# Kernel tuning notes

Measured on AMD Instinct MI355X. Metric: run time of the kernel, lower is better.

Reference implementation:

```python
import jax, jax.numpy as jnp
import numpy as np

NUM_HEADS = 8


def setup_inputs() -> dict:
    key = jax.random.key(0)
    ks = jax.random.split(key, 9)
    B, S, E = 16, 2048, 768
    s = 0.02
    return {
        "features": jax.random.normal(ks[0], (B, S, E), jnp.float32),
        "in_proj_w": jax.random.normal(ks[1], (3 * E, E), jnp.float32) * s,
        "in_proj_b": jnp.zeros((3 * E,), jnp.float32),
        "out_proj_w": jax.random.normal(ks[2], (E, E), jnp.float32) * s,
        "out_proj_b": jnp.zeros((E,), jnp.float32),
        "w1": jax.random.normal(ks[3], (384, E), jnp.float32) * s,
        "b1": jnp.zeros((384,), jnp.float32),
        "w2": jax.random.normal(ks[4], (1, 384), jnp.float32) * s,
        "b2": jnp.zeros((1,), jnp.float32),
    }


def reference(features, in_proj_w, in_proj_b, out_proj_w, out_proj_b, w1, b1, w2, b2):
    # torch nn.MultiheadAttention default batch_first=False: dim 0 is the
    # attended sequence axis (length B here), dim 1 is the MHA batch (S).
    B, S, E = features.shape
    H = NUM_HEADS
    Dh = E // H
    qkv = features @ in_proj_w.T + in_proj_b          # (B, S, 3E)
    q, k, v = jnp.split(qkv, 3, axis=-1)
    q = q.reshape(B, S, H, Dh)
    k = k.reshape(B, S, H, Dh)
    v = v.reshape(B, S, H, Dh)
    scale = 1.0 / jnp.sqrt(jnp.asarray(Dh, features.dtype))
    # attention over axis-0 positions (l, m in 0..B-1), per (s, h)
    scores = jnp.einsum('lshd,mshd->shlm', q * scale, k)
    attn = jax.nn.softmax(scores, axis=-1)
    ctx = jnp.einsum('shlm,mshd->lshd', attn, v).reshape(B, S, E)
    attn_out = ctx @ out_proj_w.T + out_proj_b        # (B, S, E)
    # batched 2-layer MLP (replaces the Python per-row loop)
    h = jax.nn.relu(attn_out @ w1.T + b1)             # (B, S, 384)
    prob = h @ w2.T + b2                              # (B, S, 1)
    contacts = jnp.broadcast_to(prob, (B, S, S))      # contacts[:, i, :] = prob[:, i]
    return contacts
```

## Files before the change

kernel.cpp:

```cpp
#include <hip/hip_runtime.h>

typedef unsigned short u16;
typedef __attribute__((ext_vector_type(8))) __bf16 bf16x8;
typedef __attribute__((ext_vector_type(4))) float floatx4;

#define B_DIM  16
#define S_DIM  2048
#define E_DIM  768
#define HEADS  8
#define DHEAD  96
#define MROWS  32768
#define QKV_LD 2304
#define NT     12

#define GLDS(gp, lp) __builtin_amdgcn_global_load_lds( \
    (const __attribute__((address_space(1))) void*)(gp), \
    (__attribute__((address_space(3))) void*)(lp), 16, 0, 0)

__device__ __forceinline__ u16 f2b(float f) {
    unsigned u = __float_as_uint(f);
    u += 0x7fffu + ((u >> 16) & 1u);
    return (u16)(u >> 16);
}
__device__ __forceinline__ float blo(unsigned u) { return __uint_as_float(u << 16); }

__device__ __forceinline__ bf16x8 ldsw(const u16* half_base, int rowh, int cb) {
    return *(const bf16x8*)((const char*)half_base + rowh * 128 + (cb ^ ((rowh & 7) << 4)));
}

#define PB0 24576
#define PB1 26304
#define PB2 26592
#define PB3 27168
#define PB4 27552
__global__ __launch_bounds__(256) void prep(const float* __restrict__ features,
                                            const float* __restrict__ in_proj_w,
                                            const float* __restrict__ w1,
                                            const float* __restrict__ out_proj_w,
                                            const float* __restrict__ bo,
                                            const float* __restrict__ b1,
                                            u16* __restrict__ fbf, u16* __restrict__ wib,
                                            u16* __restrict__ w1b, u16* __restrict__ WoT,
                                            float* __restrict__ cbuf) {
    __shared__ float tsh[32][33];
    const int b = blockIdx.x, tid = threadIdx.x;
    if (b < PB2) {
        const float* src; u16* dst; long i;
        if (b < PB0)      { src = features;  dst = fbf; i = (long)b * 256 + tid; }
        else if (b < PB1) { src = in_proj_w; dst = wib; i = (long)(b - PB0) * 256 + tid; }
        else              { src = w1;        dst = w1b; i = (long)(b - PB1) * 256 + tid; }
        float4 f = ((const float4*)src)[i];
        ushort4 r;
        r.x = f2b(f.x); r.y = f2b(f.y); r.z = f2b(f.z); r.w = f2b(f.w);
        ((ushort4*)dst)[i] = r;
    } else if (b < PB3) {
        const int t = b - PB2;
        const int bxT = t % 24, byT = t / 24;
        const int tx = tid & 31, ty = tid >> 5;
        int x = bxT * 32 + tx;
        int y = byT * 32 + ty;
#pragma unroll
        for (int j = 0; j < 4; j++) tsh[ty + j * 8][tx] = out_proj_w[(long)(y + j * 8) * 768 + x];
        __syncthreads();
        x = byT * 32 + tx;
        y = bxT * 32 + ty;
#pragma unroll
        for (int j = 0; j < 4; j++) WoT[(long)(y + j * 8) * 768 + x] = f2b(tsh[tx][ty + j * 8]);
    } else {
        const int n = b - PB3;
        const float* row = w1 + (long)n * 768;
        float s = row[tid] * bo[tid] + row[tid + 256] * bo[tid + 256] + row[tid + 512] * bo[tid + 512];
#pragma unroll
        for (int off = 32; off > 0; off >>= 1) s += __shfl_xor(s, off);
        if ((tid & 63) == 0) tsh[0][tid >> 6] = s;
        __syncthreads();
        if (tid == 0) cbuf[n] = tsh[0][0] + tsh[0][1] + tsh[0][2] + tsh[0][3] + b1[n];
    }
}

__global__ __launch_bounds__(512, 2) void qkv256(const u16* __restrict__ A,
                                                 const u16* __restrict__ W,
                                                 const float* __restrict__ bias,
                                                 u16* __restrict__ Cout,
                                                 const u16* __restrict__ gA,
                                                 const u16* __restrict__ gW,
                                                 u16* __restrict__ gC) {
    __shared__ __align__(16) u16 lds[2 * 32768];
    const int tid = threadIdx.x;
    const int bx  = blockIdx.x;
    int bm, bn, ldc, Mvalid; const u16 *Aa, *Ww; const float* bs; u16* Co; bool perm;
    if (bx < 6) {
        bn = bx % 3; bm = bx / 3;
        Aa = gA; Ww = gW; bs = nullptr; Co = gC; ldc = 768; perm = false; Mvalid = 384;
    } else {
        const int xcd = bx & 7;
        const int q   = (bx >> 3) - ((bx & 7) < 6 ? 1 : 0);
        bn = q % 9;
        bm = (q / 9) * 8 + xcd;
        Aa = A; Ww = W; bs = bias; Co = Cout; ldc = QKV_LD; perm = true; Mvalid = 1 << 30;
    }
    const int r0 = tid >> 3,        r1 = (tid + 512) >> 3;
    const int q0 = (tid & 7) ^ (r0 & 7), q1 = ((tid + 512) & 7) ^ (r1 & 7);
    const u16* pA0 = Aa + (long)(bm * 256 + r0) * 768 + q0 * 8;
    const u16* pA1 = Aa + (long)(bm * 256 + r1) * 768 + q1 * 8;
    const u16* pB0 = Ww + (long)(bn * 256 + r0) * 768 + q0 * 8;
    const u16* pB1 = Ww + (long)(bn * 256 + r1) * 768 + q1 * 8;
    u16* dA0 = lds + tid * 8;
    u16* dA1 = lds + 4096 + tid * 8;
    u16* dB0 = lds + 16384 + tid * 8;
    u16* dB1 = lds + 16384 + 4096 + tid * 8;

#define IS_A(h, p, t) do { \
    GLDS(pA0 + (h) * 98304 + (t) * 64, dA0 + (p) * 32768 + (h) * 8192); \
    GLDS(pA1 + (h) * 98304 + (t) * 64, dA1 + (p) * 32768 + (h) * 8192); } while (0)
#define IS_B(h, p, t) do { \
    GLDS(pB0 + (h) * 98304 + (t) * 64, dB0 + (p) * 32768 + (h) * 8192); \
    GLDS(pB1 + (h) * 98304 + (t) * 64, dB1 + (p) * 32768 + (h) * 8192); } while (0)
#define MFMA_PRE() do { \
    __builtin_amdgcn_s_barrier(); \
    asm volatile("s_waitcnt lgkmcnt(0)" ::: "memory"); \
    __builtin_amdgcn_sched_barrier(0); \
    __builtin_amdgcn_s_setprio(1); } while (0)
#define MFMA_POST() do { \
    __builtin_amdgcn_s_setprio(0); \
    __builtin_amdgcn_s_barrier(); } while (0)

    const int lane = tid & 63, wid = tid >> 6;
    const int wr = wid >> 2, wc = wid & 3;
    const int fr = lane & 15, fg = lane >> 4;
    const int fq2 = fg * 16;
    const int wb  = (wc & 1) * 64;
    const u16* bufA_base = lds + wr * 8192;
    const u16* bufB_base = lds + 16384 + (wc >> 1) * 8192;

    IS_A(0, 0, 0); IS_A(1, 0, 0); IS_B(0, 0, 0); IS_B(1, 0, 0);
    IS_A(0, 1, 1); IS_A(1, 1, 1);
    asm volatile("s_waitcnt vmcnt(4)" ::: "memory");
    __builtin_amdgcn_s_barrier();

    floatx4 acc[8][4] = {};
#pragma unroll 2
    for (int t = 0; t < NT; ++t) {
        const int p = t & 1, pn = p ^ 1;
        const u16* bA = bufA_base + p * 32768;
        const u16* bB = bufB_base + p * 32768;
        bf16x8 aF[4], bF[4];
#pragma unroll
        for (int i = 0; i < 4; ++i) aF[i] = ldsw(bA, i * 16 + fr, fq2);
#pragma unroll
        for (int j = 0; j < 4; ++j) bF[j] = ldsw(bB, wb + j * 16 + fr, fq2);
        if (t + 1 < NT) IS_B(0, pn, t + 1);
        MFMA_PRE();
#pragma unroll
        for (int i = 0; i < 4; ++i)
#pragma unroll
            for (int j = 0; j < 4; ++j)
                acc[i][j] = __builtin_amdgcn_mfma_f32_16x16x32_bf16(aF[i], bF[j], acc[i][j], 0, 0, 0);
        MFMA_POST();
#pragma unroll
        for (int i = 0; i < 4; ++i) aF[i] = ldsw(bA, (i + 4) * 16 + fr, fq2);
        if (t + 1 < NT) IS_B(1, pn, t + 1);
        MFMA_PRE();
#pragma unroll
        for (int i = 0; i < 4; ++i)
#pragma unroll
            for (int j = 0; j < 4; ++j)
                acc[i + 4][j] = __builtin_amdgcn_mfma_f32_16x16x32_bf16(aF[i], bF[j], acc[i + 4][j], 0, 0, 0);
        MFMA_POST();
#pragma unroll
        for (int i = 0; i < 4; ++i) aF[i] = ldsw(bA, i * 16 + fr, 64 + fq2);
#pragma unroll
        for (int j = 0; j < 4; ++j) bF[j] = ldsw(bB, wb + j * 16 + fr, 64 + fq2);
        MFMA_PRE();
#pragma unroll
        for (int i = 0; i < 4; ++i)
#pragma unroll
            for (int j = 0; j < 4; ++j)
                acc[i][j] = __builtin_amdgcn_mfma_f32_16x16x32_bf16(aF[i], bF[j], acc[i][j], 0, 0, 0);
        MFMA_POST();
#pragma unroll
        for (int i = 0; i < 4; ++i) aF[i] = ldsw(bA, (i + 4) * 16 + fr, 64 + fq2);
        MFMA_PRE();
#pragma unroll
        for (int i = 0; i < 4; ++i)
#pragma unroll
            for (int j = 0; j < 4; ++j)
                acc[i + 4][j] = __builtin_amdgcn_mfma_f32_16x16x32_bf16(aF[i], bF[j], acc[i + 4][j], 0, 0, 0);
        MFMA_POST();
        if (t + 2 < NT) {
            IS_A(0, p, t + 2); IS_A(1, p, t + 2);
            asm volatile("s_waitcnt vmcnt(4)" ::: "memory");
            __builtin_amdgcn_s_barrier();
        } else if (t + 1 < NT) {
            asm volatile("s_waitcnt vmcnt(0)" ::: "memory");
            __builtin_amdgcn_s_barrier();
        }
    }

    const int rq = fg * 4;
    float bvj[4];
#pragma unroll
    for (int j = 0; j < 4; ++j) bvj[j] = bs ? bs[bn * 256 + wc * 64 + j * 16 + fr] : 0.f;
    u16* strip = lds + wid * 2304;
    const int sr = lane >> 3, sc = lane & 7;
#pragma unroll
    for (int pass = 0; pass < 4; ++pass) {
#pragma unroll
        for (int ii = 0; ii < 2; ++ii) {
            const int i = pass * 2 + ii;
#pragma unroll
            for (int j = 0; j < 4; ++j)
#pragma unroll
                for (int r = 0; r < 4; ++r)
                    strip[(ii * 16 + rq + r) * 72 + j * 16 + fr] = f2b(acc[i][j][r] + bvj[j]);
        }
#pragma unroll
        for (int it = 0; it < 4; ++it) {
            const int lr = it * 8 + sr;
            uint4 v = *(const uint4*)(strip + lr * 72 + sc * 8);
            const int rl = bm * 256 + wr * 128 + pass * 32 + lr;
            if (rl < Mvalid) {
                const long grow = perm ? (long)(((rl & 2047) << 4) | (rl >> 11)) : (long)rl;
                *(uint4*)(Co + grow * ldc + bn * 256 + wc * 64 + sc * 8) = v;
            }
        }
    }
#undef IS_A
#undef IS_B
#undef MFMA_PRE
#undef MFMA_POST
}

__global__ __launch_bounds__(256) void attn_kernel(u16* __restrict__ qkv) {
    __shared__ __align__(16) u16 sQKV[3 * 16 * 384];
    __shared__ __align__(16) u16 sP[4][2][16][16];
    const int tid = threadIdx.x;
    const int bx  = blockIdx.x;
    const int xcd   = bx & 7;
    const int hh    = (bx >> 3) & 1;
    const int inner = bx >> 4;
    const int s = (xcd << 8) | inner;
    const u16* base = qkv + (long)s * 16 * QKV_LD + hh * 384;

#pragma unroll
    for (int it = 0; it < 9; it++) {
        const int id = it * 256 + tid;
        const int t = id / 768, within = id % 768;
        const int l = within / 48, c = within % 48;
        const int csrc = (t < 2) ? (c ^ (l & 7)) : c;
        GLDS(base + (long)l * QKV_LD + t * E_DIM + csrc * 8, sQKV + id * 8);
    }
    __syncthreads();

    const int lane = tid & 63;
    const int w    = tid >> 6;
    const int fr   = lane & 15;
    const int fg   = lane >> 4;
    floatx4 acc = {};
#pragma unroll
    for (int st = 0; st < 3; st++) {
        const int ch  = w * 12 + st * 4 + fg;
        const int chs = ch ^ (fr & 7);
        bf16x8 qa = *(const bf16x8*)(sQKV + fr * 384 + chs * 8);
        bf16x8 kb = *(const bf16x8*)(sQKV + 6144 + fr * 384 + chs * 8);
        acc = __builtin_amdgcn_mfma_f32_16x16x32_bf16(qa, kb, acc, 0, 0, 0);
    }
    const int rq = fg * 4;
#pragma unroll
    for (int r = 0; r < 4; r++) {
        float sc = acc[r] * 0.10206207261596577f;
        float mx = sc;
#pragma unroll
        for (int off = 8; off > 0; off >>= 1) mx = fmaxf(mx, __shfl_xor(mx, off));
        float e = __expf(sc - mx);
        float sum = e;
#pragma unroll
        for (int off = 8; off > 0; off >>= 1) sum += __shfl_xor(sum, off);
        const float pv = e / sum;
        const u16 phi = f2b(pv);
        const u16 plo = f2b(pv - blo((unsigned)phi));
        sP[w][0][rq + r][fr] = phi;
        sP[w][1][rq + r][fr] = plo;
    }
    __syncthreads();

    const bf16x8 pfrag = *(const bf16x8*)(&sP[w][fg >> 1][fr][(fg & 1) * 8]);
    const int mbase = (fg & 1) * 8;
    u16* ctx = sQKV;
#pragma unroll
    for (int dt = 0; dt < 6; dt++) {
        const int d = w * 96 + dt * 16 + fr;
        const u16* vcol = sQKV + 12288 + mbase * 384 + d;
        unsigned vv0 = vcol[0 * 384], vv1 = vcol[1 * 384], vv2 = vcol[2 * 384], vv3 = vcol[3 * 384];
        unsigned vv4 = vcol[4 * 384], vv5 = vcol[5 * 384], vv6 = vcol[6 * 384], vv7 = vcol[7 * 384];
        unsigned pk0 = vv0 | (vv1 << 16), pk1 = vv2 | (vv3 << 16);
        unsigned pk2 = vv4 | (vv5 << 16), pk3 = vv6 | (vv7 << 16);
        uint4 pkv = {pk0, pk1, pk2, pk3};
        bf16x8 bfrag = *(const bf16x8*)&pkv;
        floatx4 o = {};
        o = __builtin_amdgcn_mfma_f32_16x16x32_bf16(pfrag, bfrag, o, 0, 0, 0);
#pragma unroll
        for (int r = 0; r < 4; r++) ctx[(rq + r) * 384 + d] = f2b(o[r]);
    }
    __syncthreads();

#pragma unroll
    for (int j = 0; j < 3; j++) {
        const int task = j * 256 + tid;
        const int l = task / 48, c = task % 48;
        uint4 v = *(const uint4*)(sQKV + l * 384 + c * 8);
        *(uint4*)(qkv + ((long)s * 16 + l) * QKV_LD + hh * 384 + c * 8) = v;
    }
}

__global__ __launch_bounds__(256) void mlp_gemm(const u16* __restrict__ A, int lda,
                                                const u16* __restrict__ G,
                                                const float* __restrict__ cbias,
                                                const float* __restrict__ w2,
                                                float* __restrict__ part) {
    __shared__ __align__(16) u16 sA[2 * 128 * 32];
    __shared__ __align__(16) u16 sB[2 * 128 * 32];
    __shared__ float rowsum[128];
    const int tid = threadIdx.x;
    const int bx  = blockIdx.x;
    const int xcd = bx & 7;
    const int q   = bx >> 3;
    const int bn  = q % 3;
    const int t   = q / 3;
    const int bm  = (xcd << 5) | t;
    if (tid < 128) rowsum[tid] = 0.f;
    const int lane = tid & 63;
    const int wid  = tid >> 6;
    const int wm   = (wid >> 1) * 64;
    const int wn   = (wid & 1) * 64;
    const int ar = tid >> 2;
    const int ac = (tid & 3) * 8;
    const u16* Ap = A + (long)(bm * 128 + ar) * lda + ac;
    const u16* Wp = G + (long)(bn * 128 + ar) * 768 + ac;
    const long a2 = (long)64 * lda;
    const long w2s = (long)64 * 768;
    const int fr = lane & 15;
    const int fq = (lane >> 4) * 8;
    const int rq = (lane >> 4) * 4;

    floatx4 acc[4][4] = {};
    for (int k0 = 0; k0 < 768; k0 += 64) {
#pragma unroll
        for (int h = 0; h < 2; h++) {
            GLDS(Ap + k0 + h * 32,       sA + h * 4096 + tid * 8);
            GLDS(Ap + a2 + k0 + h * 32,  sA + h * 4096 + 2048 + tid * 8);
            GLDS(Wp + k0 + h * 32,       sB + h * 4096 + tid * 8);
            GLDS(Wp + w2s + k0 + h * 32, sB + h * 4096 + 2048 + tid * 8);
        }
        __syncthreads();
#pragma unroll
        for (int h = 0; h < 2; h++) {
            bf16x8 aF[4], bF[4];
#pragma unroll
            for (int i = 0; i < 4; i++) {
                aF[i] = *(const bf16x8*)(sA + h * 4096 + (wm + i * 16 + fr) * 32 + fq);
                bF[i] = *(const bf16x8*)(sB + h * 4096 + (wn + i * 16 + fr) * 32 + fq);
            }
#pragma unroll
            for (int i = 0; i < 4; i++)
#pragma unroll
                for (int j = 0; j < 4; j++)
                    acc[i][j] = __builtin_amdgcn_mfma_f32_16x16x32_bf16(aF[i], bF[j], acc[i][j], 0, 0, 0);
        }
        __syncthreads();
    }
    float partl[4][4] = {};
#pragma unroll
    for (int j = 0; j < 4; j++) {
        const int col = bn * 128 + wn + j * 16 + fr;
        const float cv = cbias[col];
        const float wv = w2[col];
#pragma unroll
        for (int i = 0; i < 4; i++)
#pragma unroll
            for (int r = 0; r < 4; r++)
                partl[i][r] += fmaxf(acc[i][j][r] + cv, 0.f) * wv;
    }
#pragma unroll
    for (int i = 0; i < 4; i++)
#pragma unroll
        for (int r = 0; r < 4; r++) {
            float v = partl[i][r];
#pragma unroll
            for (int off = 8; off > 0; off >>= 1) v += __shfl_xor(v, off);
            if (fr == 0) atomicAdd(&rowsum[wm + i * 16 + rq + r], v);
        }
    __syncthreads();
    if (tid < 128) part[(long)bn * MROWS + bm * 128 + tid] = rowsum[tid];
}

__global__ __launch_bounds__(256) void bcast_kernel(const float* __restrict__ part,
                                                    const float* __restrict__ b2,
                                                    float* __restrict__ out) {
    const int tid = threadIdx.x;
    const long s  = blockIdx.x;
    const float b2v = b2[0];
#pragma unroll
    for (int l = 0; l < 16; l++) {
        const long p = s * 16 + l;
        const float pv = part[p] + part[MROWS + p] + part[2 * MROWS + p] + b2v;
        floatx4 v4 = {pv, pv, pv, pv};
        floatx4* dst = (floatx4*)(out + ((long)l * S_DIM + s) * S_DIM);
        __builtin_nontemporal_store(v4, dst + tid);
        __builtin_nontemporal_store(v4, dst + tid + 256);
    }
}

extern "C" void kernel_launch(void* const* d_in, const int* in_sizes, int n_in,
                              void* d_out, int out_size, void* d_ws, size_t ws_size,
                              hipStream_t stream) {
    const float* features   = (const float*)d_in[0];
    const float* in_proj_b  = (const float*)d_in[2];
    const float* out_proj_b = (const float*)d_in[4];
    const float* b1 = (const float*)d_in[6];
    const float* w2 = (const float*)d_in[7];
    const float* b2 = (const float*)d_in[8];
    float* out = (float*)d_out;

    char* p = (char*)d_ws;
    u16* fbf = (u16*)p; p += (size_t)MROWS * E_DIM * 2;
    u16* wib = (u16*)p; p += (size_t)QKV_LD * E_DIM * 2;
    u16* w1b = (u16*)p; p += (size_t)384 * E_DIM * 2;
    u16* WoT = (u16*)p; p += (size_t)E_DIM * E_DIM * 2;
    u16* Gbf = (u16*)p; p += (size_t)384 * E_DIM * 2;
    float* cbuf  = (float*)p; p += 384 * 4;
    float* partb = (float*)p; p += (size_t)3 * MROWS * 4;
    p = (char*)(((size_t)p + 255) & ~(size_t)255);
    u16* qkv = (u16*)p; p += (size_t)MROWS * QKV_LD * 2;
    u16* ctx = qkv;

    prep<<<PB4, 256, 0, stream>>>(features, (const float*)d_in[1], (const float*)d_in[5],
                                  (const float*)d_in[3], out_proj_b, b1,
                                  fbf, wib, w1b, WoT, cbuf);
    qkv256<<<1158, 512, 0, stream>>>(fbf, wib, in_proj_b, qkv, w1b, WoT, Gbf);
    attn_kernel<<<S_DIM * 2, 256, 0, stream>>>(qkv);
    mlp_gemm<<<768, 256, 0, stream>>>(ctx, QKV_LD, Gbf, cbuf, w2, partb);
    bcast_kernel<<<S_DIM, 256, 0, stream>>>(partb, b2, out);
}
```

Baseline: 548.6 us.

## Replace MLP GEMM with 256x256-tile pipelined kernel using swizzled LDS

```diff
diff --git a/kernel.cpp b/kernel.cpp
--- a/kernel.cpp
+++ b/kernel.cpp
@@ -313,85 +313,149 @@
     }
 }
 
-__global__ __launch_bounds__(256) void mlp_gemm(const u16* __restrict__ A, int lda,
-                                                const u16* __restrict__ G,
-                                                const float* __restrict__ cbias,
-                                                const float* __restrict__ w2,
-                                                float* __restrict__ part) {
-    __shared__ __align__(16) u16 sA[2 * 128 * 32];
-    __shared__ __align__(16) u16 sB[2 * 128 * 32];
-    __shared__ float rowsum[128];
+__global__ __launch_bounds__(512, 2) void mlp256(const u16* __restrict__ A,
+                                                 const u16* __restrict__ G,
+                                                 const float* __restrict__ cbias,
+                                                 const float* __restrict__ w2,
+                                                 float* __restrict__ part) {
+    __shared__ __align__(16) u16 lds[2 * 32768];
+    __shared__ float rowsum[256];
     const int tid = threadIdx.x;
     const int bx  = blockIdx.x;
     const int xcd = bx & 7;
     const int q   = bx >> 3;
-    const int bn  = q % 3;
-    const int t   = q / 3;
-    const int bm  = (xcd << 5) | t;
-    if (tid < 128) rowsum[tid] = 0.f;
-    const int lane = tid & 63;
-    const int wid  = tid >> 6;
-    const int wm   = (wid >> 1) * 64;
-    const int wn   = (wid & 1) * 64;
-    const int ar = tid >> 2;
-    const int ac = (tid & 3) * 8;
-    const u16* Ap = A + (long)(bm * 128 + ar) * lda + ac;
-    const u16* Wp = G + (long)(bn * 128 + ar) * 768 + ac;
-    const long a2 = (long)64 * lda;
-    const long w2s = (long)64 * 768;
-    const int fr = lane & 15;
-    const int fq = (lane >> 4) * 8;
-    const int rq = (lane >> 4) * 4;
-
-    floatx4 acc[4][4] = {};
-    for (int k0 = 0; k0 < 768; k0 += 64) {
-#pragma unroll
-        for (int h = 0; h < 2; h++) {
-            GLDS(Ap + k0 + h * 32,       sA + h * 4096 + tid * 8);
-            GLDS(Ap + a2 + k0 + h * 32,  sA + h * 4096 + 2048 + tid * 8);
-            GLDS(Wp + k0 + h * 32,       sB + h * 4096 + tid * 8);
-            GLDS(Wp + w2s + k0 + h * 32, sB + h * 4096 + 2048 + tid * 8);
+    const int bm  = xcd * 16 + (q >> 1);
+    const int bn  = q & 1;
+    const int r0 = tid >> 3,        r1 = (tid + 512) >> 3;
+    const int q0 = (tid & 7) ^ (r0 & 7), q1 = ((tid + 512) & 7) ^ (r1 & 7);
+    const u16* pA0 = A + (long)(bm * 256 + r0) * QKV_LD + q0 * 8;
+    const u16* pA1 = A + (long)(bm * 256 + r1) * QKV_LD + q1 * 8;
+    const u16* pB0 = G + (long)(bn * 256 + r0) * 768 + q0 * 8;
+    const u16* pB1 = G + (long)(bn * 256 + r1) * 768 + q1 * 8;
+    u16* dA0 = lds + tid * 8;
+    u16* dA1 = lds + 4096 + tid * 8;
+    u16* dB0 = lds + 16384 + tid * 8;
+    u16* dB1 = lds + 16384 + 4096 + tid * 8;
+
+#define IS_A(h, p, t) do { \
+    GLDS(pA0 + (h) * (128L * QKV_LD) + (t) * 64, dA0 + (p) * 32768 + (h) * 8192); \
+    GLDS(pA1 + (h) * (128L * QKV_LD) + (t) * 64, dA1 + (p) * 32768 + (h) * 8192); } while (0)
+#define IS_B(h, p, t) do { \
+    GLDS(pB0 + (h) * 98304 + (t) * 64, dB0 + (p) * 32768 + (h) * 8192); \
+    GLDS(pB1 + (h) * 98304 + (t) * 64, dB1 + (p) * 32768 + (h) * 8192); } while (0)
+#define MFMA_PRE() do { \
+    __builtin_amdgcn_s_barrier(); \
+    asm volatile("s_waitcnt lgkmcnt(0)" ::: "memory"); \
+    __builtin_amdgcn_sched_barrier(0); \
+    __builtin_amdgcn_s_setprio(1); } while (0)
+#define MFMA_POST() do { \
+    __builtin_amdgcn_s_setprio(0); \
+    __builtin_amdgcn_s_barrier(); } while (0)
+
+    const int lane = tid & 63, wid = tid >> 6;
+    const int wr = wid >> 2, wc = wid & 3;
+    const int fr = lane & 15, fg = lane >> 4;
+    const int fq2 = fg * 16;
+    const int wb  = (wc & 1) * 64;
+    const u16* bufA_base = lds + wr * 8192;
+    const u16* bufB_base = lds + 16384 + (wc >> 1) * 8192;
+
+    IS_A(0, 0, 0); IS_A(1, 0, 0); IS_B(0, 0, 0); IS_B(1, 0, 0);
+    IS_A(0, 1, 1); IS_A(1, 1, 1);
+    asm volatile("s_waitcnt vmcnt(4)" ::: "memory");
+    __builtin_amdgcn_s_barrier();
+
+    floatx4 acc[8][4] = {};
+#pragma unroll 2
+    for (int t = 0; t < NT; ++t) {
+        const int p = t & 1, pn = p ^ 1;
+        const u16* bA = bufA_base + p * 32768;
+        const u16* bB = bufB_base + p * 32768;
+        bf16x8 aF[4], bF[4];
+#pragma unroll
+        for (int i = 0; i < 4; ++i) aF[i] = ldsw(bA, i * 16 + fr, fq2);
+#pragma unroll
+        for (int j = 0; j < 4; ++j) bF[j] = ldsw(bB, wb + j * 16 + fr, fq2);
+        if (t + 1 < NT) IS_B(0, pn, t + 1);
+        MFMA_PRE();
+#pragma unroll
+        for (int i = 0; i < 4; ++i)
+#pragma unroll
+            for (int j = 0; j < 4; ++j)
+                acc[i][j] = __builtin_amdgcn_mfma_f32_16x16x32_bf16(aF[i], bF[j], acc[i][j], 0, 0, 0);
+        MFMA_POST();
+#pragma unroll
+        for (int i = 0; i < 4; ++i) aF[i] = ldsw(bA, (i + 4) * 16 + fr, fq2);
+        if (t + 1 < NT) IS_B(1, pn, t + 1);
+        MFMA_PRE();
+#pragma unroll
+        for (int i = 0; i < 4; ++i)
+#pragma unroll
+            for (int j = 0; j < 4; ++j)
+                acc[i + 4][j] = __builtin_amdgcn_mfma_f32_16x16x32_bf16(aF[i], bF[j], acc[i + 4][j], 0, 0, 0);
+        MFMA_POST();
+#pragma unroll
+        for (int i = 0; i < 4; ++i) aF[i] = ldsw(bA, i * 16 + fr, 64 + fq2);
+#pragma unroll
+        for (int j = 0; j < 4; ++j) bF[j] = ldsw(bB, wb + j * 16 + fr, 64 + fq2);
+        MFMA_PRE();
+#pragma unroll
+        for (int i = 0; i < 4; ++i)
+#pragma unroll
+            for (int j = 0; j < 4; ++j)
+                acc[i][j] = __builtin_amdgcn_mfma_f32_16x16x32_bf16(aF[i], bF[j], acc[i][j], 0, 0, 0);
+        MFMA_POST();
+#pragma unroll
+        for (int i = 0; i < 4; ++i) aF[i] = ldsw(bA, (i + 4) * 16 + fr, 64 + fq2);
+        MFMA_PRE();
+#pragma unroll
+        for (int i = 0; i < 4; ++i)
+#pragma unroll
+            for (int j = 0; j < 4; ++j)
+                acc[i + 4][j] = __builtin_amdgcn_mfma_f32_16x16x32_bf16(aF[i], bF[j], acc[i + 4][j], 0, 0, 0);
+        MFMA_POST();
+        if (t + 2 < NT) {
+            IS_A(0, p, t + 2); IS_A(1, p, t + 2);
+            asm volatile("s_waitcnt vmcnt(4)" ::: "memory");
+            __builtin_amdgcn_s_barrier();
+        } else if (t + 1 < NT) {
+            asm volatile("s_waitcnt vmcnt(0)" ::: "memory");
+            __builtin_amdgcn_s_barrier();
         }
-        __syncthreads();
-#pragma unroll
-        for (int h = 0; h < 2; h++) {
-            bf16x8 aF[4], bF[4];
-#pragma unroll
-            for (int i = 0; i < 4; i++) {
-                aF[i] = *(const bf16x8*)(sA + h * 4096 + (wm + i * 16 + fr) * 32 + fq);
-                bF[i] = *(const bf16x8*)(sB + h * 4096 + (wn + i * 16 + fr) * 32 + fq);
+    }
+
+    if (tid < 256) rowsum[tid] = 0.f;
+    __syncthreads();
+    float partl[8][4] = {};
+#pragma unroll
+    for (int j = 0; j < 4; ++j) {
+        const int col = bn * 256 + wc * 64 + j * 16 + fr;
+        const bool valid = col < 384;
+        const float cv = valid ? cbias[col] : 0.f;
+        const float wv = valid ? w2[col] : 0.f;
+#pragma unroll
+        for (int i = 0; i < 8; ++i)
+#pragma unroll
+            for (int r = 0; r < 4; ++r) {
+                const float c2 = fmaxf(acc[i][j][r] + cv, 0.f) * wv;
+                partl[i][r] += valid ? c2 : 0.f;
             }
-#pragma unroll
-            for (int i = 0; i < 4; i++)
-#pragma unroll
-                for (int j = 0; j < 4; j++)
-                    acc[i][j] = __builtin_amdgcn_mfma_f32_16x16x32_bf16(aF[i], bF[j], acc[i][j], 0, 0, 0);
-        }
-        __syncthreads();
-    }
-    float partl[4][4] = {};
-#pragma unroll
-    for (int j = 0; j < 4; j++) {
-        const int col = bn * 128 + wn + j * 16 + fr;
-        const float cv = cbias[col];
-        const float wv = w2[col];
-#pragma unroll
-        for (int i = 0; i < 4; i++)
-#pragma unroll
-            for (int r = 0; r < 4; r++)
-                partl[i][r] += fmaxf(acc[i][j][r] + cv, 0.f) * wv;
-    }
-#pragma unroll
-    for (int i = 0; i < 4; i++)
-#pragma unroll
-        for (int r = 0; r < 4; r++) {
+    }
+#pragma unroll
+    for (int i = 0; i < 8; ++i)
+#pragma unroll
+        for (int r = 0; r < 4; ++r) {
             float v = partl[i][r];
 #pragma unroll
             for (int off = 8; off > 0; off >>= 1) v += __shfl_xor(v, off);
-            if (fr == 0) atomicAdd(&rowsum[wm + i * 16 + rq + r], v);
+            if (fr == 0) atomicAdd(&rowsum[wr * 128 + i * 16 + fg * 4 + r], v);
         }
     __syncthreads();
-    if (tid < 128) part[(long)bn * MROWS + bm * 128 + tid] = rowsum[tid];
+    if (tid < 256) part[(long)bn * MROWS + bm * 256 + tid] = rowsum[tid];
+#undef IS_A
+#undef IS_B
+#undef MFMA_PRE
+#undef MFMA_POST
 }
 
 __global__ __launch_bounds__(256) void bcast_kernel(const float* __restrict__ part,
@@ -403,7 +467,7 @@
 #pragma unroll
     for (int l = 0; l < 16; l++) {
         const long p = s * 16 + l;
-        const float pv = part[p] + part[MROWS + p] + part[2 * MROWS + p] + b2v;
+        const float pv = part[p] + part[MROWS + p] + b2v;
         floatx4 v4 = {pv, pv, pv, pv};
         floatx4* dst = (floatx4*)(out + ((long)l * S_DIM + s) * S_DIM);
         __builtin_nontemporal_store(v4, dst + tid);
@@ -427,9 +491,9 @@
     u16* wib = (u16*)p; p += (size_t)QKV_LD * E_DIM * 2;
     u16* w1b = (u16*)p; p += (size_t)384 * E_DIM * 2;
     u16* WoT = (u16*)p; p += (size_t)E_DIM * E_DIM * 2;
-    u16* Gbf = (u16*)p; p += (size_t)384 * E_DIM * 2;
+    u16* Gbf = (u16*)p; p += (size_t)512 * E_DIM * 2;
     float* cbuf  = (float*)p; p += 384 * 4;
-    float* partb = (float*)p; p += (size_t)3 * MROWS * 4;
+    float* partb = (float*)p; p += (size_t)2 * MROWS * 4;
     p = (char*)(((size_t)p + 255) & ~(size_t)255);
     u16* qkv = (u16*)p; p += (size_t)MROWS * QKV_LD * 2;
     u16* ctx = qkv;
@@ -439,6 +503,6 @@
                                   fbf, wib, w1b, WoT, cbuf);
     qkv256<<<1158, 512, 0, stream>>>(fbf, wib, in_proj_b, qkv, w1b, WoT, Gbf);
     attn_kernel<<<S_DIM * 2, 256, 0, stream>>>(qkv);
-    mlp_gemm<<<768, 256, 0, stream>>>(ctx, QKV_LD, Gbf, cbuf, w2, partb);
+    mlp256<<<256, 512, 0, stream>>>(ctx, Gbf, cbuf, w2, partb);
     bcast_kernel<<<S_DIM, 256, 0, stream>>>(partb, b2, out);
 }
```

After: 546.3 us. About the same (-0.4%).
